# Kernel optimization log

Hardware: AMD Instinct MI355X
Metric: run time of the kernel (lower is better)

The kernel has to match this reference:

```python
import jax, jax.numpy as jnp
import numpy as np

N, IN_F, OUT_F = 2048, 512, 512

def setup_inputs() -> dict:
    key = jax.random.key(0)
    kx, ka, kb = jax.random.split(key, 3)
    x = jax.random.uniform(kx, (N, IN_F), dtype=jnp.float32)          # inputs in [0,1]
    a = jax.random.uniform(ka, (OUT_F, IN_F), dtype=jnp.float32)      # weight in [0,1]
    b = jax.random.uniform(kb, (OUT_F,), dtype=jnp.float32)           # bias in [0,1]
    return {"x": x, "a": a, "b": b}

def reference(x, a, b):
    # Lukasiewicz / max-plus 'matmul':
    # y[n,o] = max(0, max_i(x[n,i] + a[o,i] - 1)), then max with bias b[o].
    inter = x[:, None, :] + a[None, :, :] - 1.0        # [N, out, in]
    y = jnp.maximum(jnp.max(inter, axis=-1), 0.0)      # [N, out]
    y = jnp.maximum(y, b[None, :])
    return y
```

## Files before the change

kernel.cpp:

```cpp
#include <hip/hip_runtime.h>
#include <cstdint>


#define NROW 2048
#define NK   512
#define NCOL 512
#define RPB  16
#define CBL  256
#define KQ   8
typedef float f32x4 __attribute__((ext_vector_type(4)));

__device__ __forceinline__ void async_load16(const float* g, float* l) {
  __builtin_amdgcn_global_load_lds(
      (const __attribute__((address_space(1))) void*)g,
      (__attribute__((address_space(3))) void*)l, 16, 0, 0);
}

__global__ __launch_bounds__(256) void luka_prep(const float* __restrict__ A,
                                                 f32x4* __restrict__ Apb) {
  int idx = blockIdx.x * 256 + threadIdx.x;
  int o  = idx >> 7;
  int k4 = idx & 127;
  f32x4 v = *(const f32x4*)(A + o * NK + k4 * 4);
  Apb[(((o >> 8) * 128) + k4) * 256 + (o & 255)] = v;
}

__global__ __launch_bounds__(1024, 4) void luka_main(
    const f32x4* __restrict__ Apb, const float* __restrict__ X,
    const float* __restrict__ Bv, float* __restrict__ Y) {
  __shared__ float lds[RPB * NK];
  __shared__ float red[16 * 4 * CBL];
  const int tid  = threadIdx.x;
  const int lane = tid & 63;
  const int w    = tid >> 6;
  const int colblk  = blockIdx.x;
  const int rowBase = blockIdx.y * RPB;

  {
    const float* Xg = X + (size_t)rowBase * NK;
#pragma unroll
    for (int rnd = 0; rnd < 2; ++rnd) {
      int base = rnd * 1024 + w * 64;
      async_load16(Xg + (size_t)(base + lane) * 4, &lds[base * 4]);
    }
  }

  const f32x4* __restrict__ Aw =
      Apb + ((size_t)(colblk * 128 + w * KQ) * 256 + lane);

  float acc[RPB][4];
#pragma unroll
  for (int r = 0; r < RPB; ++r)
#pragma unroll
    for (int c = 0; c < 4; ++c) acc[r][c] = 0.0f;

  __syncthreads();

#pragma unroll
  for (int j = 0; j < KQ; ++j) {
    f32x4 a0 = Aw[j * 256];
    f32x4 a1 = Aw[j * 256 + 64];
    f32x4 a2 = Aw[j * 256 + 128];
    f32x4 a3 = Aw[j * 256 + 192];
    const int kb = (w * KQ + j) * 4;
#pragma unroll
    for (int r = 0; r < RPB; ++r) {
      const f32x4 xv = *(const f32x4*)&lds[r * NK + kb];
      f32x4 s0 = a0 + xv;
      f32x4 s1 = a1 + xv;
      f32x4 s2 = a2 + xv;
      f32x4 s3 = a3 + xv;
      acc[r][0] = fmaxf(fmaxf(s0.x, s0.y), acc[r][0]);
      acc[r][0] = fmaxf(fmaxf(s0.z, s0.w), acc[r][0]);
      acc[r][1] = fmaxf(fmaxf(s1.x, s1.y), acc[r][1]);
      acc[r][1] = fmaxf(fmaxf(s1.z, s1.w), acc[r][1]);
      acc[r][2] = fmaxf(fmaxf(s2.x, s2.y), acc[r][2]);
      acc[r][2] = fmaxf(fmaxf(s2.z, s2.w), acc[r][2]);
      acc[r][3] = fmaxf(fmaxf(s3.x, s3.y), acc[r][3]);
      acc[r][3] = fmaxf(fmaxf(s3.z, s3.w), acc[r][3]);
    }
  }

  const int rc = tid >> 8;
  const int cc = tid & 255;
  const float bv = Bv[colblk * CBL + cc];
#pragma unroll
  for (int p = 0; p < 4; ++p) {
#pragma unroll
    for (int r2 = 0; r2 < 4; ++r2)
#pragma unroll
      for (int c = 0; c < 4; ++c)
        red[(w * 4 + r2) * CBL + c * 64 + lane] = acc[p * 4 + r2][c];
    __syncthreads();
    float m = red[rc * CBL + cc];
#pragma unroll
    for (int ww = 1; ww < 16; ++ww)
      m = fmaxf(m, red[(ww * 4 + rc) * CBL + cc]);
    float t = m - 1.0f;
    Y[(size_t)(rowBase + p * 4 + rc) * NCOL + colblk * CBL + cc] =
        fmaxf(fmaxf(t, bv), 0.0f);
    __syncthreads();
  }
}

#define TILE 64
#define BK   64
__global__ __launch_bounds__(256) void luka_fb(
    const float* __restrict__ X, const float* __restrict__ A,
    const float* __restrict__ Bv, float* __restrict__ Y) {
  __shared__ float xs[2][TILE * BK];
  __shared__ float as[2][TILE * BK];
  const int tid = threadIdx.x, wave = tid >> 6, tx = tid & 15, ty = tid >> 4;
  const int rowBase = blockIdx.y * TILE, colBase = blockIdx.x * TILE;
  uint32_t xoff[4], aoff[4];
#pragma unroll
  for (int r = 0; r < 4; ++r) {
    int row = ty * 4 + r;
    xoff[r] = (uint32_t)row * 256u + ((uint32_t)((row & 15) ^ (row >> 2)) << 4);
  }
#pragma unroll
  for (int c = 0; c < 4; ++c) {
    int row = tx * 4 + c;
    aoff[c] = (uint32_t)row * 256u + ((uint32_t)((row & 15) ^ (row >> 2)) << 4);
  }
  float acc[4][4];
#pragma unroll
  for (int r = 0; r < 4; ++r)
#pragma unroll
    for (int c = 0; c < 4; ++c) acc[r][c] = 0.0f;
  const int row0 = tid >> 4, sl = tid & 15;
  auto stage = [&](int buf, int kt) {
#pragma unroll
    for (int j = 0; j < 4; ++j) {
      int row = row0 + j * 16;
      int m = (row & 15) ^ (row >> 2);
      int kk = ((sl ^ m) << 2);
      async_load16(X + (size_t)(rowBase + row) * NK + kt * BK + kk,
                   &xs[buf][j * 1024 + wave * 256]);
      async_load16(A + (size_t)(colBase + row) * NK + kt * BK + kk,
                   &as[buf][j * 1024 + wave * 256]);
    }
  };
  stage(0, 0);
  __syncthreads();
  int buf = 0;
#pragma unroll 1
  for (int kt = 0; kt < NK / BK; ++kt) {
    if (kt < NK / BK - 1) stage(buf ^ 1, kt + 1);
    const char* xb = (const char*)&xs[buf][0];
    const char* ab = (const char*)&as[buf][0];
#pragma unroll
    for (int s4 = 0; s4 < BK / 4; ++s4) {
      f32x4 xf[4], af[4];
#pragma unroll
      for (int r = 0; r < 4; ++r)
        xf[r] = *(const f32x4*)(xb + (xoff[r] ^ (uint32_t)(s4 << 4)));
#pragma unroll
      for (int c = 0; c < 4; ++c)
        af[c] = *(const f32x4*)(ab + (aoff[c] ^ (uint32_t)(s4 << 4)));
#pragma unroll
      for (int r = 0; r < 4; ++r)
#pragma unroll
        for (int c = 0; c < 4; ++c) {
          f32x4 s = xf[r] + af[c];
          float t0 = fmaxf(fmaxf(s.x, s.y), acc[r][c]);
          acc[r][c] = fmaxf(fmaxf(s.z, s.w), t0);
        }
    }
    __syncthreads();
    buf ^= 1;
  }
  const f32x4 bv = *(const f32x4*)&Bv[colBase + tx * 4];
  float bvv[4] = {bv.x, bv.y, bv.z, bv.w};
#pragma unroll
  for (int r = 0; r < 4; ++r) {
    f32x4 o;
    o.x = fmaxf(fmaxf(acc[r][0] - 1.0f, bvv[0]), 0.0f);
    o.y = fmaxf(fmaxf(acc[r][1] - 1.0f, bvv[1]), 0.0f);
    o.z = fmaxf(fmaxf(acc[r][2] - 1.0f, bvv[2]), 0.0f);
    o.w = fmaxf(fmaxf(acc[r][3] - 1.0f, bvv[3]), 0.0f);
    *(f32x4*)&Y[(size_t)(rowBase + ty * 4 + r) * NCOL + colBase + tx * 4] = o;
  }
}

extern "C" void kernel_launch(void* const* d_in, const int* in_sizes, int n_in,
                              void* d_out, int out_size, void* d_ws, size_t ws_size,
                              hipStream_t stream) {
  const float* X = (const float*)d_in[0];
  const float* A = (const float*)d_in[1];
  const float* B = (const float*)d_in[2];
  float* Y = (float*)d_out;

  if (ws_size >= (size_t)NCOL * NK * sizeof(float)) {
    f32x4* Apb = (f32x4*)d_ws;
    luka_prep<<<dim3(NCOL * NK / 4 / 256), dim3(256), 0, stream>>>(A, Apb);
    dim3 grid(NCOL / CBL, NROW / RPB);
    luka_main<<<grid, dim3(1024), 0, stream>>>(Apb, X, B, Y);
  } else {
    dim3 grid(NCOL / TILE, NROW / TILE);
    luka_fb<<<grid, dim3(256), 0, stream>>>(X, A, B, Y);
  }
}
```

Baseline: 85.58 us.

## Shrink main kernel to 256-thread blocks with 8 rows and register-prefetched weights

Reshapes the main kernel from 1024-thread blocks of 16 rows into 256-thread blocks of 8 rows. Each of the 4 waves now covers a quarter of K (32 chunks instead of 8), so the cross-wave reduction shrinks to a 4-way max done with a single barrier. Weight vectors for the next K step are loaded into registers during the current step to hide global load latency. The grid doubles in rows, so weight reuse per block is halved and each wave runs a longer serial loop.

New measurement: 83.75 us. 2.1% less time.

```diff
diff --git a/kernel.cpp b/kernel.cpp
--- a/kernel.cpp
+++ b/kernel.cpp
@@ -5,9 +5,9 @@
 #define NROW 2048
 #define NK   512
 #define NCOL 512
-#define RPB  16
+#define RPB  8
 #define CBL  256
-#define KQ   8
+#define KQ   32
 typedef float f32x4 __attribute__((ext_vector_type(4)));
 
 __device__ __forceinline__ void async_load16(const float* g, float* l) {
@@ -25,11 +25,11 @@
   Apb[(((o >> 8) * 128) + k4) * 256 + (o & 255)] = v;
 }
 
-__global__ __launch_bounds__(1024, 4) void luka_main(
+__global__ __launch_bounds__(256, 2) void luka_main(
     const f32x4* __restrict__ Apb, const float* __restrict__ X,
     const float* __restrict__ Bv, float* __restrict__ Y) {
-  __shared__ float lds[RPB * NK];
-  __shared__ float red[16 * 4 * CBL];
+  __shared__ float xsl[RPB * NK];
+  __shared__ float red[4 * RPB * CBL];
   const int tid  = threadIdx.x;
   const int lane = tid & 63;
   const int w    = tid >> 6;
@@ -39,9 +39,9 @@
   {
     const float* Xg = X + (size_t)rowBase * NK;
 #pragma unroll
-    for (int rnd = 0; rnd < 2; ++rnd) {
-      int base = rnd * 1024 + w * 64;
-      async_load16(Xg + (size_t)(base + lane) * 4, &lds[base * 4]);
+    for (int rnd = 0; rnd < 4; ++rnd) {
+      int base = rnd * 256 + w * 64;
+      async_load16(Xg + (size_t)(base + lane) * 4, &xsl[base * 4]);
     }
   }
 
@@ -54,18 +54,23 @@
 #pragma unroll
     for (int c = 0; c < 4; ++c) acc[r][c] = 0.0f;
 
+  f32x4 a0 = Aw[0], a1 = Aw[64], a2 = Aw[128], a3 = Aw[192];
+
   __syncthreads();
 
-#pragma unroll
+#pragma unroll 2
   for (int j = 0; j < KQ; ++j) {
-    f32x4 a0 = Aw[j * 256];
-    f32x4 a1 = Aw[j * 256 + 64];
-    f32x4 a2 = Aw[j * 256 + 128];
-    f32x4 a3 = Aw[j * 256 + 192];
+    f32x4 n0, n1, n2, n3;
+    if (j + 1 < KQ) {
+      n0 = Aw[(j + 1) * 256];
+      n1 = Aw[(j + 1) * 256 + 64];
+      n2 = Aw[(j + 1) * 256 + 128];
+      n3 = Aw[(j + 1) * 256 + 192];
+    }
     const int kb = (w * KQ + j) * 4;
 #pragma unroll
     for (int r = 0; r < RPB; ++r) {
-      const f32x4 xv = *(const f32x4*)&lds[r * NK + kb];
+      const f32x4 xv = *(const f32x4*)&xsl[r * NK + kb];
       f32x4 s0 = a0 + xv;
       f32x4 s1 = a1 + xv;
       f32x4 s2 = a2 + xv;
@@ -79,27 +84,26 @@
       acc[r][3] = fmaxf(fmaxf(s3.x, s3.y), acc[r][3]);
       acc[r][3] = fmaxf(fmaxf(s3.z, s3.w), acc[r][3]);
     }
-  }
-
-  const int rc = tid >> 8;
-  const int cc = tid & 255;
-  const float bv = Bv[colblk * CBL + cc];
-#pragma unroll
-  for (int p = 0; p < 4; ++p) {
-#pragma unroll
-    for (int r2 = 0; r2 < 4; ++r2)
-#pragma unroll
-      for (int c = 0; c < 4; ++c)
-        red[(w * 4 + r2) * CBL + c * 64 + lane] = acc[p * 4 + r2][c];
-    __syncthreads();
-    float m = red[rc * CBL + cc];
-#pragma unroll
-    for (int ww = 1; ww < 16; ++ww)
-      m = fmaxf(m, red[(ww * 4 + rc) * CBL + cc]);
+    a0 = n0; a1 = n1; a2 = n2; a3 = n3;
+  }
+
+#pragma unroll
+  for (int r = 0; r < RPB; ++r)
+#pragma unroll
+    for (int c = 0; c < 4; ++c)
+      red[(w * RPB + r) * CBL + c * 64 + lane] = acc[r][c];
+  __syncthreads();
+
+  const float bv = Bv[colblk * CBL + tid];
+#pragma unroll
+  for (int p = 0; p < RPB; ++p) {
+    float m = fmaxf(fmaxf(red[(0 * RPB + p) * CBL + tid],
+                          red[(1 * RPB + p) * CBL + tid]),
+                    fmaxf(red[(2 * RPB + p) * CBL + tid],
+                          red[(3 * RPB + p) * CBL + tid]));
     float t = m - 1.0f;
-    Y[(size_t)(rowBase + p * 4 + rc) * NCOL + colblk * CBL + cc] =
+    Y[(size_t)(rowBase + p) * NCOL + colblk * CBL + tid] =
         fmaxf(fmaxf(t, bv), 0.0f);
-    __syncthreads();
   }
 }
 
@@ -195,7 +199,7 @@
     f32x4* Apb = (f32x4*)d_ws;
     luka_prep<<<dim3(NCOL * NK / 4 / 256), dim3(256), 0, stream>>>(A, Apb);
     dim3 grid(NCOL / CBL, NROW / RPB);
-    luka_main<<<grid, dim3(1024), 0, stream>>>(Apb, X, B, Y);
+    luka_main<<<grid, dim3(256), 0, stream>>>(Apb, X, B, Y);
   } else {
     dim3 grid(NCOL / TILE, NROW / TILE);
     luka_fb<<<grid, dim3(256), 0, stream>>>(X, A, B, Y);
```
